# Performance work log

Measured on AMD Instinct MI355X. Metric: run time of the kernel, lower is better.

## Reference

```python
import jax, jax.numpy as jnp
import numpy as np

B, C, N, D, F = 2048, 64, 64, 64, 128  # batch, cin_hidden, num_features, embed_dim, feature_maps


def setup_inputs() -> dict:
    key = jax.random.key(0)
    k1, k2, k3 = jax.random.split(key, 3)
    xj = jax.random.normal(k1, (B, C, D), dtype=jnp.float32)
    x0 = jax.random.normal(k2, (B, N, D), dtype=jnp.float32)
    # xavier_uniform_ on (F, C, N): fan_in = C*N? torch treats dim1 as fan_in-ish;
    # exact init distribution is irrelevant for correctness testing, use scaled uniform.
    limit = float(np.sqrt(6.0 / (C + N)))
    W = jax.random.uniform(k3, (F, C, N), dtype=jnp.float32, minval=-limit, maxval=limit)
    return {"xj": xj, "x0": x0, "W": W}


def reference(xj, x0, W):
    # Original: hadamard[b,c,n,d] = x0[b,n,d]*xj[b,c,d];
    # out[b,f,c,d] = sum_n hadamard * W[f,c,n]; cin_out = sum_c out; cin_p_out = sum_d cin_out.
    # Fused: cin_out[b,f,d] = sum_{c,n} W[f,c,n] * xj[b,c,d] * x0[b,n,d]
    cin_out = jnp.einsum('bcd,bnd,fcn->bfd', xj, x0, W)  # (B, F, D)
    cin_p_out = jnp.sum(cin_out, axis=-1)  # (B, F)
    return (cin_out, cin_p_out)
```

## Files before the change

### kernel.cpp

```cpp
#include <hip/hip_runtime.h>


typedef unsigned short u16;
typedef __attribute__((ext_vector_type(8))) short bf16x8;
typedef __attribute__((ext_vector_type(4))) short bf16x4;
typedef __attribute__((ext_vector_type(4))) float f32x4;

__device__ __forceinline__ u16 f2b(float f) {
  union { float f; unsigned u; } x; x.f = f;
  unsigned r = x.u + 0x7fffu + ((x.u >> 16) & 1u);
  return (u16)(r >> 16);
}
__device__ __forceinline__ float b2f_lo(unsigned u) {
  union { unsigned u; float f; } x; x.u = u << 16; return x.f;
}
__device__ __forceinline__ float b2f_hi(unsigned u) {
  union { unsigned u; float f; } x; x.u = u & 0xffff0000u; return x.f;
}
__device__ __forceinline__ int swz(int row, int col) {
  return (col & 7) | ((((col >> 3) ^ row) & 7) << 3);
}

__global__ __launch_bounds__(256) void wconv_kernel(const float* __restrict__ W,
                                                    u16* __restrict__ Wb) {
  int i = (blockIdx.x * 256 + threadIdx.x) * 8;
  const float4 a = *(const float4*)(W + i);
  const float4 b = *(const float4*)(W + i + 4);
  bf16x8 r;
  r[0] = (short)f2b(a.x); r[1] = (short)f2b(a.y);
  r[2] = (short)f2b(a.z); r[3] = (short)f2b(a.w);
  r[4] = (short)f2b(b.x); r[5] = (short)f2b(b.y);
  r[6] = (short)f2b(b.z); r[7] = (short)f2b(b.w);
  *(bf16x8*)(Wb + i) = r;
}

__global__ __launch_bounds__(256) void cin_kernel(
    const float* __restrict__ xj, const float* __restrict__ x0,
    const u16* __restrict__ Wb, float* __restrict__ out, float* __restrict__ pout) {
  extern __shared__ u16 smem[];
  u16* x0T = smem;
  u16* xjN = smem + 8192;
  u16* Wt  = smem + 16384;

  const int t  = threadIdx.x;
  const int b0 = blockIdx.x * 2;

  for (int bb = 0; bb < 2; ++bb) {
    const float* s0 = x0 + (size_t)(b0 + bb) * 4096;
    const float* sj = xj + (size_t)(b0 + bb) * 4096;
#pragma unroll
    for (int p = 0; p < 4; ++p) {
      const int e = p * 1024 + t * 4;
      const int r = e >> 6, d = e & 63;
      const float4 v0 = *(const float4*)(s0 + e);
      const float4 vj = *(const float4*)(sj + e);
      x0T[bb * 4096 + (d + 0) * 64 + swz(d + 0, r)] = f2b(v0.x);
      x0T[bb * 4096 + (d + 1) * 64 + swz(d + 1, r)] = f2b(v0.y);
      x0T[bb * 4096 + (d + 2) * 64 + swz(d + 2, r)] = f2b(v0.z);
      x0T[bb * 4096 + (d + 3) * 64 + swz(d + 3, r)] = f2b(v0.w);
      bf16x4 jr;
      jr[0] = (short)f2b(vj.x); jr[1] = (short)f2b(vj.y);
      jr[2] = (short)f2b(vj.z); jr[3] = (short)f2b(vj.w);
      *(bf16x4*)&xjN[bb * 4096 + r * 64 + d] = jr;
    }
  }
  __syncthreads();

  const int wid = t >> 6, lane = t & 63;
  const int wr = wid >> 1, wc = wid & 1;
  const int lr = lane & 15, lg = lane >> 4;

  bf16x8 af[4][2];
#pragma unroll
  for (int mf = 0; mf < 4; ++mf)
#pragma unroll
    for (int kk = 0; kk < 2; ++kk) {
      const int d = mf * 16 + lr;
      af[mf][kk] = *(const bf16x8*)&x0T[wr * 4096 + d * 64 + swz(d, kk * 32 + lg * 8)];
    }

  f32x4 acc[4][4];
#pragma unroll
  for (int i = 0; i < 4; ++i)
#pragma unroll
    for (int j = 0; j < 4; ++j) acc[i][j] = (f32x4){0.f, 0.f, 0.f, 0.f};

  bf16x8 wreg[4];
#pragma unroll
  for (int q = 0; q < 4; ++q) {
    const int e = q * 2048 + t * 8;
    wreg[q] = *(const bf16x8*)(Wb + (size_t)(e >> 6) * 4096 + (e & 63));
  }

  for (int c = 0; c < 64; ++c) {
    u16* wbuf = Wt + (c & 1) * 8192;
#pragma unroll
    for (int q = 0; q < 4; ++q) {
      const int e = q * 2048 + t * 8;
      *(bf16x8*)&wbuf[(e >> 6) * 64 + swz(e >> 6, e & 63)] = wreg[q];
    }
    if (c < 63) {
#pragma unroll
      for (int q = 0; q < 4; ++q) {
        const int e = q * 2048 + t * 8;
        wreg[q] = *(const bf16x8*)(Wb + (size_t)(e >> 6) * 4096 + (c + 1) * 64 + (e & 63));
      }
    }
    __syncthreads();

    bf16x8 bfv[4][2];
#pragma unroll
    for (int nf = 0; nf < 4; ++nf)
#pragma unroll
      for (int kk = 0; kk < 2; ++kk) {
        const int row = wc * 64 + nf * 16 + lr;
        bfv[nf][kk] = *(const bf16x8*)&wbuf[row * 64 + swz(row, kk * 32 + lg * 8)];
      }

#pragma unroll
    for (int mf = 0; mf < 4; ++mf) {
      f32x4 z[4];
#pragma unroll
      for (int nf = 0; nf < 4; ++nf) {
        f32x4 zz = (f32x4){0.f, 0.f, 0.f, 0.f};
        zz = __builtin_amdgcn_mfma_f32_16x16x32_bf16(af[mf][0], bfv[nf][0], zz, 0, 0, 0);
        zz = __builtin_amdgcn_mfma_f32_16x16x32_bf16(af[mf][1], bfv[nf][1], zz, 0, 0, 0);
        z[nf] = zz;
      }
      const int d4 = mf * 16 + lg * 4;
      const bf16x4 xv = *(const bf16x4*)&xjN[wr * 4096 + c * 64 + d4];
      union { bf16x4 v; unsigned u[2]; } uu; uu.v = xv;
      const float xjf0 = b2f_lo(uu.u[0]), xjf1 = b2f_hi(uu.u[0]);
      const float xjf2 = b2f_lo(uu.u[1]), xjf3 = b2f_hi(uu.u[1]);
#pragma unroll
      for (int nf = 0; nf < 4; ++nf) {
        acc[mf][nf][0] += xjf0 * z[nf][0];
        acc[mf][nf][1] += xjf1 * z[nf][1];
        acc[mf][nf][2] += xjf2 * z[nf][2];
        acc[mf][nf][3] += xjf3 * z[nf][3];
      }
    }
  }

  const int b = b0 + wr;
  float psum[4] = {0.f, 0.f, 0.f, 0.f};
#pragma unroll
  for (int mf = 0; mf < 4; ++mf) {
    const int d = mf * 16 + lg * 4;
#pragma unroll
    for (int nf = 0; nf < 4; ++nf) {
      const int f = wc * 64 + nf * 16 + lr;
      const f32x4 v = acc[mf][nf];
      *(f32x4*)(out + (size_t)b * (128 * 64) + (size_t)f * 64 + d) = v;
      psum[nf] += v[0] + v[1] + v[2] + v[3];
    }
  }
#pragma unroll
  for (int nf = 0; nf < 4; ++nf) {
    float s = psum[nf];
    s += __shfl_xor(s, 16, 64);
    s += __shfl_xor(s, 32, 64);
    if (lg == 0) pout[(size_t)b * 128 + wc * 64 + nf * 16 + lr] = s;
  }
}

extern "C" void kernel_launch(void* const* d_in, const int* in_sizes, int n_in,
                              void* d_out, int out_size, void* d_ws, size_t ws_size,
                              hipStream_t stream) {
  const float* xj = (const float*)d_in[0];
  const float* x0 = (const float*)d_in[1];
  const float* W  = (const float*)d_in[2];
  float* out  = (float*)d_out;
  float* pout = out + (size_t)2048 * 128 * 64;
  u16* Wb = (u16*)d_ws;

  wconv_kernel<<<256, 256, 0, stream>>>(W, Wb);
  cin_kernel<<<1024, 256, 65536, stream>>>(xj, x0, Wb, out, pout);
}
```

Before: 173.5 us.

## Fold xj scaling into MFMA A operand and stream W directly into registers

The kernel now scales x0 by xj[c,d] in fp32 before the bf16 conversion, so the MFMA accumulates straight into acc and the separate per-c scalar multiply-add pass goes away. W tiles and xj values are loaded from global memory into double-buffered registers, which removes the shared-memory W staging and the per-iteration __syncthreads. x0 is kept in fp32 LDS (32KB) and the launch bound asks for 2 blocks per CU. The cost is more VALU work per c, with 16 bf16 conversions per mf, plus redundant global loads of W across waves and higher register pressure.

```diff
diff --git a/kernel.cpp b/kernel.cpp
--- a/kernel.cpp
+++ b/kernel.cpp
@@ -1,9 +1,9 @@
 #include <hip/hip_runtime.h>
+#include <hip/hip_bf16.h>
 
 
 typedef unsigned short u16;
 typedef __attribute__((ext_vector_type(8))) short bf16x8;
-typedef __attribute__((ext_vector_type(4))) short bf16x4;
 typedef __attribute__((ext_vector_type(4))) float f32x4;
 
 __device__ __forceinline__ u16 f2b(float f) {
@@ -11,14 +11,8 @@
   unsigned r = x.u + 0x7fffu + ((x.u >> 16) & 1u);
   return (u16)(r >> 16);
 }
-__device__ __forceinline__ float b2f_lo(unsigned u) {
-  union { unsigned u; float f; } x; x.u = u << 16; return x.f;
-}
-__device__ __forceinline__ float b2f_hi(unsigned u) {
-  union { unsigned u; float f; } x; x.u = u & 0xffff0000u; return x.f;
-}
-__device__ __forceinline__ int swz(int row, int col) {
-  return (col & 7) | ((((col >> 3) ^ row) & 7) << 3);
+__device__ __forceinline__ u16 cvb(float f) {
+  return __bfloat16_as_ushort(__float2bfloat16(f));
 }
 
 __global__ __launch_bounds__(256) void wconv_kernel(const float* __restrict__ W,
@@ -34,34 +28,26 @@
   *(bf16x8*)(Wb + i) = r;
 }
 
-__global__ __launch_bounds__(256) void cin_kernel(
+__global__ __launch_bounds__(256, 2) void cin_kernel(
     const float* __restrict__ xj, const float* __restrict__ x0,
     const u16* __restrict__ Wb, float* __restrict__ out, float* __restrict__ pout) {
-  extern __shared__ u16 smem[];
-  u16* x0T = smem;
-  u16* xjN = smem + 8192;
-  u16* Wt  = smem + 16384;
+  __shared__ float x0T[2][64][64];
 
   const int t  = threadIdx.x;
   const int b0 = blockIdx.x * 2;
 
   for (int bb = 0; bb < 2; ++bb) {
     const float* s0 = x0 + (size_t)(b0 + bb) * 4096;
-    const float* sj = xj + (size_t)(b0 + bb) * 4096;
 #pragma unroll
     for (int p = 0; p < 4; ++p) {
       const int e = p * 1024 + t * 4;
-      const int r = e >> 6, d = e & 63;
-      const float4 v0 = *(const float4*)(s0 + e);
-      const float4 vj = *(const float4*)(sj + e);
-      x0T[bb * 4096 + (d + 0) * 64 + swz(d + 0, r)] = f2b(v0.x);
-      x0T[bb * 4096 + (d + 1) * 64 + swz(d + 1, r)] = f2b(v0.y);
-      x0T[bb * 4096 + (d + 2) * 64 + swz(d + 2, r)] = f2b(v0.z);
-      x0T[bb * 4096 + (d + 3) * 64 + swz(d + 3, r)] = f2b(v0.w);
-      bf16x4 jr;
-      jr[0] = (short)f2b(vj.x); jr[1] = (short)f2b(vj.y);
-      jr[2] = (short)f2b(vj.z); jr[3] = (short)f2b(vj.w);
-      *(bf16x4*)&xjN[bb * 4096 + r * 64 + d] = jr;
+      const int n = e >> 6, d0 = e & 63;
+      const float4 v = *(const float4*)(s0 + e);
+      const int ch = n >> 2, sub = n & 3;
+      x0T[bb][d0 + 0][(((ch ^ (d0 + 0)) & 15) << 2) | sub] = v.x;
+      x0T[bb][d0 + 1][(((ch ^ (d0 + 1)) & 15) << 2) | sub] = v.y;
+      x0T[bb][d0 + 2][(((ch ^ (d0 + 2)) & 15) << 2) | sub] = v.z;
+      x0T[bb][d0 + 3][(((ch ^ (d0 + 3)) & 15) << 2) | sub] = v.w;
     }
   }
   __syncthreads();
@@ -70,14 +56,16 @@
   const int wr = wid >> 1, wc = wid & 1;
   const int lr = lane & 15, lg = lane >> 4;
 
-  bf16x8 af[4][2];
+  f32x4 af4[4][4];
 #pragma unroll
-  for (int mf = 0; mf < 4; ++mf)
+  for (int mf = 0; mf < 4; ++mf) {
+    const int d = mf * 16 + lr;
 #pragma unroll
-    for (int kk = 0; kk < 2; ++kk) {
-      const int d = mf * 16 + lr;
-      af[mf][kk] = *(const bf16x8*)&x0T[wr * 4096 + d * 64 + swz(d, kk * 32 + lg * 8)];
+    for (int q = 0; q < 4; ++q) {
+      const int ch = (q >> 1) * 8 + lg * 2 + (q & 1);
+      af4[mf][q] = *(const f32x4*)&x0T[wr][d][((ch ^ d) & 15) << 2];
     }
+  }
 
   f32x4 acc[4][4];
 #pragma unroll
@@ -85,61 +73,57 @@
 #pragma unroll
     for (int j = 0; j < 4; ++j) acc[i][j] = (f32x4){0.f, 0.f, 0.f, 0.f};
 
-  bf16x8 wreg[4];
+  const u16* wbase = Wb + (size_t)(wc * 64 + lr) * 4096 + lg * 8;
+  const float* xjp = xj + (size_t)(b0 + wr) * 4096;
+
+  bf16x8 wbuf[2][4][2];
+  float  xjb[2][4];
+
 #pragma unroll
-  for (int q = 0; q < 4; ++q) {
-    const int e = q * 2048 + t * 8;
-    wreg[q] = *(const bf16x8*)(Wb + (size_t)(e >> 6) * 4096 + (e & 63));
-  }
+  for (int nf = 0; nf < 4; ++nf)
+#pragma unroll
+    for (int kk = 0; kk < 2; ++kk)
+      wbuf[0][nf][kk] = *(const bf16x8*)(wbase + nf * 65536 + kk * 32);
+#pragma unroll
+  for (int mf = 0; mf < 4; ++mf) xjb[0][mf] = xjp[mf * 16 + lr];
 
-  for (int c = 0; c < 64; ++c) {
-    u16* wbuf = Wt + (c & 1) * 8192;
-#pragma unroll
-    for (int q = 0; q < 4; ++q) {
-      const int e = q * 2048 + t * 8;
-      *(bf16x8*)&wbuf[(e >> 6) * 64 + swz(e >> 6, e & 63)] = wreg[q];
-    }
-    if (c < 63) {
-#pragma unroll
-      for (int q = 0; q < 4; ++q) {
-        const int e = q * 2048 + t * 8;
-        wreg[q] = *(const bf16x8*)(Wb + (size_t)(e >> 6) * 4096 + (c + 1) * 64 + (e & 63));
-      }
-    }
-    __syncthreads();
-
-    bf16x8 bfv[4][2];
+  auto body = [&](int c, int cur, int nxt) {
+    const int cn = (c < 63) ? c + 1 : c;
 #pragma unroll
     for (int nf = 0; nf < 4; ++nf)
 #pragma unroll
-      for (int kk = 0; kk < 2; ++kk) {
-        const int row = wc * 64 + nf * 16 + lr;
-        bfv[nf][kk] = *(const bf16x8*)&wbuf[row * 64 + swz(row, kk * 32 + lg * 8)];
-      }
+      for (int kk = 0; kk < 2; ++kk)
+        wbuf[nxt][nf][kk] = *(const bf16x8*)(wbase + nf * 65536 + cn * 64 + kk * 32);
+#pragma unroll
+    for (int mf = 0; mf < 4; ++mf) xjb[nxt][mf] = xjp[cn * 64 + mf * 16 + lr];
 
 #pragma unroll
     for (int mf = 0; mf < 4; ++mf) {
-      f32x4 z[4];
+      const float xf = xjb[cur][mf];
+      bf16x8 ap[2];
 #pragma unroll
-      for (int nf = 0; nf < 4; ++nf) {
-        f32x4 zz = (f32x4){0.f, 0.f, 0.f, 0.f};
-        zz = __builtin_amdgcn_mfma_f32_16x16x32_bf16(af[mf][0], bfv[nf][0], zz, 0, 0, 0);
-        zz = __builtin_amdgcn_mfma_f32_16x16x32_bf16(af[mf][1], bfv[nf][1], zz, 0, 0, 0);
-        z[nf] = zz;
+      for (int kk = 0; kk < 2; ++kk) {
+        const f32x4 pa = xf * af4[mf][kk * 2 + 0];
+        const f32x4 pb = xf * af4[mf][kk * 2 + 1];
+        bf16x8 r;
+        r[0] = (short)cvb(pa[0]); r[1] = (short)cvb(pa[1]);
+        r[2] = (short)cvb(pa[2]); r[3] = (short)cvb(pa[3]);
+        r[4] = (short)cvb(pb[0]); r[5] = (short)cvb(pb[1]);
+        r[6] = (short)cvb(pb[2]); r[7] = (short)cvb(pb[3]);
+        ap[kk] = r;
       }
-      const int d4 = mf * 16 + lg * 4;
-      const bf16x4 xv = *(const bf16x4*)&xjN[wr * 4096 + c * 64 + d4];
-      union { bf16x4 v; unsigned u[2]; } uu; uu.v = xv;
-      const float xjf0 = b2f_lo(uu.u[0]), xjf1 = b2f_hi(uu.u[0]);
-      const float xjf2 = b2f_lo(uu.u[1]), xjf3 = b2f_hi(uu.u[1]);
 #pragma unroll
-      for (int nf = 0; nf < 4; ++nf) {
-        acc[mf][nf][0] += xjf0 * z[nf][0];
-        acc[mf][nf][1] += xjf1 * z[nf][1];
-        acc[mf][nf][2] += xjf2 * z[nf][2];
-        acc[mf][nf][3] += xjf3 * z[nf][3];
-      }
+      for (int kk = 0; kk < 2; ++kk)
+#pragma unroll
+        for (int nf = 0; nf < 4; ++nf)
+          acc[mf][nf] = __builtin_amdgcn_mfma_f32_16x16x32_bf16(
+              ap[kk], wbuf[cur][nf][kk], acc[mf][nf], 0, 0, 0);
     }
+  };
+
+  for (int cc = 0; cc < 32; ++cc) {
+    body(2 * cc + 0, 0, 1);
+    body(2 * cc + 1, 1, 0);
   }
 
   const int b = b0 + wr;
@@ -175,5 +159,5 @@
   u16* Wb = (u16*)d_ws;
 
   wconv_kernel<<<256, 256, 0, stream>>>(W, Wb);
-  cin_kernel<<<1024, 256, 65536, stream>>>(xj, x0, Wb, out, pout);
+  cin_kernel<<<1024, 256, 0, stream>>>(xj, x0, Wb, out, pout);
 }
```

New measurement: 251.9 us. 45.2% more time.
